# Optimization experiments

Measured on AMD Instinct MI355X. Metric: run time of the kernel, lower is better.

The kernel has to match this reference:

```python
import jax, jax.numpy as jnp
import numpy as np

INPUT_DIM, LATENT_DIM, HIDDEN_DIM, BATCH = 1024, 128, 1024, 32768


def setup_inputs() -> dict:
    key = jax.random.key(0)
    ks = jax.random.split(key, 12)
    s = 0.02
    x = (jax.random.uniform(ks[0], (BATCH, INPUT_DIM)) < 0.5).astype(jnp.float32)  # binary data
    eps = jax.random.normal(ks[1], (BATCH, LATENT_DIM), dtype=jnp.float32)
    return {
        "x": x,
        "eps": eps,
        "We1": jax.random.normal(ks[2], (INPUT_DIM, HIDDEN_DIM)) * s,
        "be1": jnp.zeros((HIDDEN_DIM,), jnp.float32),
        "Wmu": jax.random.normal(ks[3], (HIDDEN_DIM, LATENT_DIM)) * s,
        "bmu": jnp.zeros((LATENT_DIM,), jnp.float32),
        "Wls": jax.random.normal(ks[4], (HIDDEN_DIM, LATENT_DIM)) * s,
        "bls": jnp.zeros((LATENT_DIM,), jnp.float32),
        "Wd1": jax.random.normal(ks[5], (LATENT_DIM, HIDDEN_DIM)) * s,
        "bd1": jnp.zeros((HIDDEN_DIM,), jnp.float32),
        "Wd2": jax.random.normal(ks[6], (HIDDEN_DIM, INPUT_DIM)) * s,
        "bd2": jnp.zeros((INPUT_DIM,), jnp.float32),
    }


def reference(x, eps, We1, be1, Wmu, bmu, Wls, bls, Wd1, bd1, Wd2, bd2):
    # Encoder: one hidden ReLU layer, mu / logsigma heads
    h = jax.nn.relu(x @ We1 + be1)                      # [B, H]
    mu = h @ Wmu + bmu                                  # [B, L]
    logsigma = h @ Wls + bls                            # [B, L]
    # Reparameterization: z = sigma * eps + mu (vectorized diag(exp(logsigma)) @ eps)
    z = mu + jnp.exp(logsigma) * eps                    # [B, L]
    # Decoder: one hidden ReLU layer, sigmoid Bernoulli params
    hd = jax.nn.relu(z @ Wd1 + bd1)                     # [B, H]
    theta = jax.nn.sigmoid(hd @ Wd2 + bd2)              # [B, D]
    # Bernoulli log-likelihood: sum_j log(theta^x * (1-theta)^(1-x))
    log_px = jnp.sum(x * jnp.log(theta) + (1.0 - x) * jnp.log1p(-theta), axis=-1)  # [B]
    # KL(q||N(0,I)) = 0.5 * sum(sigma^2 + mu^2 - log(sigma^2) - 1)
    kl = 0.5 * jnp.sum(jnp.exp(2.0 * logsigma) + mu * mu - 2.0 * logsigma - 1.0, axis=-1)  # [B]
    return log_px - kl                                  # elbo_mc [B]
```

## Files before the change

kernel.cpp:

```cpp
#include <hip/hip_runtime.h>
#include <cstdint>
#include <cstddef>


typedef __bf16 bf16x8 __attribute__((ext_vector_type(8)));
typedef float f32x4 __attribute__((ext_vector_type(4)));

__device__ __forceinline__ unsigned short f32_to_bf16(float f) {
  unsigned int u = __float_as_uint(f);
  u += 0x7fffu + ((u >> 16) & 1u);
  return (unsigned short)(u >> 16);
}

__global__ void cast_bf16_k(const float* __restrict__ in,
                            unsigned short* __restrict__ out, int n4) {
  int stride = gridDim.x * blockDim.x;
  for (int i = blockIdx.x * blockDim.x + threadIdx.x; i < n4; i += stride) {
    float4 v = reinterpret_cast<const float4*>(in)[i];
    ushort4 o = make_ushort4(f32_to_bf16(v.x), f32_to_bf16(v.y),
                             f32_to_bf16(v.z), f32_to_bf16(v.w));
    reinterpret_cast<ushort4*>(out)[i] = o;
  }
}

struct TransJob { const float* in; unsigned short* out; int K, N, blkEnd; };

__global__ void transpose_all_k(TransJob j0, TransJob j1, TransJob j2,
                                TransJob j3, TransJob j4) {
  __shared__ float tile[32][33];
  int bid = blockIdx.x;
  TransJob j; int base;
  if (bid < j0.blkEnd)      { j = j0; base = 0; }
  else if (bid < j1.blkEnd) { j = j1; base = j0.blkEnd; }
  else if (bid < j2.blkEnd) { j = j2; base = j1.blkEnd; }
  else if (bid < j3.blkEnd) { j = j3; base = j2.blkEnd; }
  else                      { j = j4; base = j3.blkEnd; }
  int local = bid - base;
  int gxN = j.N >> 5;
  int n0 = (local % gxN) * 32, k0 = (local / gxN) * 32;
  int tx = threadIdx.x, ty = threadIdx.y;
#pragma unroll
  for (int r = 0; r < 32; r += 8)
    tile[ty + r][tx] = j.in[(size_t)(k0 + ty + r) * j.N + n0 + tx];
  __syncthreads();
#pragma unroll
  for (int r = 0; r < 32; r += 8)
    j.out[(size_t)(n0 + ty + r) * j.K + k0 + tx] = f32_to_bf16(tile[tx][ty + r]);
}

__device__ __forceinline__ void gl_lds16(const unsigned short* g, unsigned short* l) {
  __builtin_amdgcn_global_load_lds(
      (__attribute__((address_space(1))) void*)g,
      (__attribute__((address_space(3))) void*)l, 16, 0, 0);
}

template <int EPI>
__global__ __launch_bounds__(512, 2) void gemm256(
    const unsigned short* __restrict__ A, const unsigned short* __restrict__ BT,
    int gx, int N, int K,
    const float* __restrict__ bias0,
    unsigned short* __restrict__ outb, float* __restrict__ outf,
    const unsigned short* __restrict__ xbf) {
  __shared__ __align__(16) unsigned short lds[2][2][256 * 64];

  const int tid = threadIdx.x;
  const int lane = tid & 63;
  const int wave = tid >> 6;
  const int wr = wave >> 2;
  const int wc = wave & 3;
  const int lm = lane & 15, lq = lane >> 4;
  const int sw = lm & 7;

  const int bid = blockIdx.x;
  const int xcd = bid & 7;
  const int t8 = bid >> 3;
  const int m0 = (xcd + 8 * (t8 / gx)) * 256;
  const int n0 = (t8 % gx) * 256;
  const int NT = K >> 6;

  const unsigned short* gpA[2];
  const unsigned short* gpB[2];
  int loA[2], loB[2];
#pragma unroll
  for (int r = 0; r < 2; ++r) {
    int c = tid + 512 * r, rl = c >> 3, q8 = c & 7;
    int rowA = (rl & 63) + ((rl >> 6) << 7);
    int rowB = (rl & 31) + ((rl >> 5) << 6);
    gpA[r] = A + (size_t)(m0 + rowA) * K + (q8 ^ (rowA & 7)) * 8;
    gpB[r] = BT + (size_t)(n0 + rowB) * K + (q8 ^ (rowB & 7)) * 8;
    loA[r] = rowA * 64 + q8 * 8;
    loB[r] = rowB * 64 + q8 * 8;
  }

  auto stage = [&](int kind, int buf, int kt) {
#pragma unroll
    for (int r = 0; r < 2; ++r) {
      if (kind == 0)      gl_lds16(gpA[r] + kt * 64,          &lds[buf][0][loA[r]]);
      else if (kind == 3) gl_lds16(gpA[r] + 64 * K + kt * 64, &lds[buf][0][loA[r] + 64 * 64]);
      else if (kind == 1) gl_lds16(gpB[r] + kt * 64,          &lds[buf][1][loB[r]]);
      else                gl_lds16(gpB[r] + 32 * K + kt * 64, &lds[buf][1][loB[r] + 32 * 64]);
    }
  };

  stage(0, 0, 0); stage(1, 0, 0); stage(2, 0, 0); stage(3, 0, 0);
  stage(0, 1, 1); stage(1, 1, 1); stage(2, 1, 1);
  asm volatile("s_waitcnt vmcnt(6)" ::: "memory");
  __builtin_amdgcn_s_barrier();

  f32x4 acc[8][4] = {};

  const int aRow = (wr * 128 + lm) * 64;
  const int bRow = (wc * 64 + lm) * 64;
  const int c0 = ((0 | lq) ^ sw) * 8;
  const int c1 = ((4 | lq) ^ sw) * 8;

  for (int t = 0; t < NT; ++t) {
    const int b = t & 1;
    const unsigned short* Ab = &lds[b][0][0];
    const unsigned short* Bb = &lds[b][1][0];
    bf16x8 af[4][2], bf1[2][2], bf2[2][2];

#pragma unroll
    for (int i = 0; i < 4; ++i) {
      af[i][0] = *reinterpret_cast<const bf16x8*>(Ab + aRow + i * 16 * 64 + c0);
      af[i][1] = *reinterpret_cast<const bf16x8*>(Ab + aRow + i * 16 * 64 + c1);
    }
#pragma unroll
    for (int j = 0; j < 2; ++j) {
      bf1[j][0] = *reinterpret_cast<const bf16x8*>(Bb + bRow + j * 16 * 64 + c0);
      bf1[j][1] = *reinterpret_cast<const bf16x8*>(Bb + bRow + j * 16 * 64 + c1);
    }
    if (t + 1 < NT) stage(3, (t + 1) & 1, t + 1);
    __builtin_amdgcn_s_barrier();
    asm volatile("s_waitcnt lgkmcnt(0)" ::: "memory");
    __builtin_amdgcn_s_setprio(1);
#pragma unroll
    for (int s = 0; s < 2; ++s)
#pragma unroll
      for (int i = 0; i < 4; ++i)
#pragma unroll
        for (int j = 0; j < 2; ++j)
          acc[i][j] = __builtin_amdgcn_mfma_f32_16x16x32_bf16(af[i][s], bf1[j][s], acc[i][j], 0, 0, 0);
    __builtin_amdgcn_s_setprio(0);
    __builtin_amdgcn_s_barrier();

#pragma unroll
    for (int j = 0; j < 2; ++j) {
      bf2[j][0] = *reinterpret_cast<const bf16x8*>(Bb + bRow + (j + 2) * 16 * 64 + c0);
      bf2[j][1] = *reinterpret_cast<const bf16x8*>(Bb + bRow + (j + 2) * 16 * 64 + c1);
    }
    if (t + 2 < NT) stage(0, b, t + 2);
    __builtin_amdgcn_s_barrier();
    asm volatile("s_waitcnt lgkmcnt(0)" ::: "memory");
    __builtin_amdgcn_s_setprio(1);
#pragma unroll
    for (int s = 0; s < 2; ++s)
#pragma unroll
      for (int i = 0; i < 4; ++i)
#pragma unroll
        for (int j = 0; j < 2; ++j)
          acc[i][j + 2] = __builtin_amdgcn_mfma_f32_16x16x32_bf16(af[i][s], bf2[j][s], acc[i][j + 2], 0, 0, 0);
    __builtin_amdgcn_s_setprio(0);
    __builtin_amdgcn_s_barrier();

#pragma unroll
    for (int i = 0; i < 4; ++i) {
      af[i][0] = *reinterpret_cast<const bf16x8*>(Ab + aRow + (64 + i * 16) * 64 + c0);
      af[i][1] = *reinterpret_cast<const bf16x8*>(Ab + aRow + (64 + i * 16) * 64 + c1);
    }
    if (t + 2 < NT) stage(1, b, t + 2);
    __builtin_amdgcn_s_barrier();
    asm volatile("s_waitcnt lgkmcnt(0)" ::: "memory");
    __builtin_amdgcn_s_setprio(1);
#pragma unroll
    for (int s = 0; s < 2; ++s)
#pragma unroll
      for (int i = 0; i < 4; ++i)
#pragma unroll
        for (int j = 0; j < 2; ++j)
          acc[i + 4][j] = __builtin_amdgcn_mfma_f32_16x16x32_bf16(af[i][s], bf1[j][s], acc[i + 4][j], 0, 0, 0);
    __builtin_amdgcn_s_setprio(0);
    __builtin_amdgcn_s_barrier();

    if (t + 2 < NT) stage(2, b, t + 2);
    __builtin_amdgcn_s_barrier();
    __builtin_amdgcn_s_setprio(1);
#pragma unroll
    for (int s = 0; s < 2; ++s)
#pragma unroll
      for (int i = 0; i < 4; ++i)
#pragma unroll
        for (int j = 0; j < 2; ++j)
          acc[i + 4][j + 2] = __builtin_amdgcn_mfma_f32_16x16x32_bf16(af[i][s], bf2[j][s], acc[i + 4][j + 2], 0, 0, 0);
    __builtin_amdgcn_s_setprio(0);
    if (t + 2 < NT)      { asm volatile("s_waitcnt vmcnt(6)" ::: "memory"); }
    else if (t + 1 < NT) { asm volatile("s_waitcnt vmcnt(0)" ::: "memory"); }
    __builtin_amdgcn_s_barrier();
  }

  if (EPI == 0) {
#pragma unroll
    for (int i = 0; i < 8; ++i)
#pragma unroll
      for (int j = 0; j < 4; ++j) {
        int col = n0 + wc * 64 + j * 16 + lm;
        float bias = bias0[col];
#pragma unroll
        for (int r = 0; r < 4; ++r) {
          int row = m0 + wr * 128 + i * 16 + lq * 4 + r;
          float v = acc[i][j][r] + bias;
          outb[(size_t)row * N + col] = f32_to_bf16(fmaxf(v, 0.f));
        }
      }
  } else {
#pragma unroll
    for (int i = 0; i < 8; ++i) {
      float rs[4] = {0.f, 0.f, 0.f, 0.f};
#pragma unroll
      for (int j = 0; j < 4; ++j) {
        int col = n0 + wc * 64 + j * 16 + lm;
        float bias = bias0[col];
#pragma unroll
        for (int r = 0; r < 4; ++r) {
          int row = m0 + wr * 128 + i * 16 + lq * 4 + r;
          float l = acc[i][j][r] + bias;
          unsigned short xb = xbf[(size_t)row * N + col];
          float tt = xb ? -l : l;
          float sp = fmaxf(tt, 0.f) + __logf(1.f + __expf(-fabsf(tt)));
          rs[r] -= sp;
        }
      }
#pragma unroll
      for (int off = 1; off < 16; off <<= 1)
#pragma unroll
        for (int r = 0; r < 4; ++r) rs[r] += __shfl_xor(rs[r], off, 64);
      if (lm == 0) {
#pragma unroll
        for (int r = 0; r < 4; ++r)
          atomicAdd(&outf[m0 + wr * 128 + i * 16 + lq * 4 + r], rs[r]);
      }
    }
  }
}

__global__ __launch_bounds__(256, 1) void gemm2_zkl(
    const unsigned short* __restrict__ A,
    const unsigned short* __restrict__ BT,
    int K,
    const float* __restrict__ bmu, const float* __restrict__ bls,
    const float* __restrict__ eps,
    unsigned short* __restrict__ z,
    float* __restrict__ out) {
  __shared__ __align__(16) unsigned short As[128 * 64];
  __shared__ __align__(16) unsigned short Bs[256 * 64];

  const int tid = threadIdx.x;
  const int lane = tid & 63;
  const int wave = tid >> 6;
  const int m0 = blockIdx.x * 128;
  const int lm = lane & 15, lq = lane >> 4;

  const unsigned short* agp[4];
  const unsigned short* bgp[8];
#pragma unroll
  for (int r = 0; r < 4; ++r) {
    int c = tid + 256 * r;
    int row = c >> 3, q = (c & 7) ^ (row & 7);
    agp[r] = A + (size_t)(m0 + row) * K + q * 8;
  }
#pragma unroll
  for (int r = 0; r < 8; ++r) {
    int c = tid + 256 * r;
    int row = c >> 3, q = (c & 7) ^ (row & 7);
    bgp[r] = BT + (size_t)row * K + q * 8;
  }
  const int sw = lm & 7;

  f32x4 acc[2][16] = {};

  for (int kt = 0; kt < K; kt += 64) {
#pragma unroll
    for (int r = 0; r < 4; ++r) gl_lds16(agp[r] + kt, As + (tid + 256 * r) * 8);
#pragma unroll
    for (int r = 0; r < 8; ++r) gl_lds16(bgp[r] + kt, Bs + (tid + 256 * r) * 8);
    __syncthreads();

#pragma unroll
    for (int s = 0; s < 2; ++s) {
      const int so = ((s << 2) | lq) ^ sw;
      bf16x8 af[2];
#pragma unroll
      for (int i = 0; i < 2; ++i)
        af[i] = *reinterpret_cast<const bf16x8*>(As + (wave * 32 + i * 16 + lm) * 64 + so * 8);
#pragma unroll
      for (int j = 0; j < 16; ++j) {
        bf16x8 b = *reinterpret_cast<const bf16x8*>(Bs + (j * 16 + lm) * 64 + so * 8);
        acc[0][j] = __builtin_amdgcn_mfma_f32_16x16x32_bf16(af[0], b, acc[0][j], 0, 0, 0);
        acc[1][j] = __builtin_amdgcn_mfma_f32_16x16x32_bf16(af[1], b, acc[1][j], 0, 0, 0);
      }
    }
    __syncthreads();
  }

#pragma unroll
  for (int i = 0; i < 2; ++i) {
    float kl[4] = {0.f, 0.f, 0.f, 0.f};
#pragma unroll
    for (int j = 0; j < 8; ++j) {
      int dim = j * 16 + lm;
      float bm = bmu[dim], bl = bls[dim];
#pragma unroll
      for (int r = 0; r < 4; ++r) {
        int row = m0 + wave * 32 + i * 16 + lq * 4 + r;
        float mu = acc[i][j][r] + bm;
        float ls = acc[i][j + 8][r] + bl;
        float e = eps[(size_t)row * 128 + dim];
        z[(size_t)row * 128 + dim] = f32_to_bf16(fmaf(__expf(ls), e, mu));
        kl[r] += 0.5f * (__expf(2.f * ls) + mu * mu - 2.f * ls - 1.f);
      }
    }
#pragma unroll
    for (int off = 1; off < 16; off <<= 1)
#pragma unroll
      for (int r = 0; r < 4; ++r) kl[r] += __shfl_xor(kl[r], off, 64);
    if (lm == 0) {
#pragma unroll
      for (int r = 0; r < 4; ++r)
        out[m0 + wave * 32 + i * 16 + lq * 4 + r] = -kl[r];
    }
  }
}

extern "C" void kernel_launch(void* const* d_in, const int* in_sizes, int n_in,
                              void* d_out, int out_size, void* d_ws, size_t ws_size,
                              hipStream_t stream) {
  const float* x   = (const float*)d_in[0];
  const float* eps = (const float*)d_in[1];
  const float* We1 = (const float*)d_in[2];
  const float* be1 = (const float*)d_in[3];
  const float* Wmu = (const float*)d_in[4];
  const float* bmu = (const float*)d_in[5];
  const float* Wls = (const float*)d_in[6];
  const float* bls = (const float*)d_in[7];
  const float* Wd1 = (const float*)d_in[8];
  const float* bd1 = (const float*)d_in[9];
  const float* Wd2 = (const float*)d_in[10];
  const float* bd2 = (const float*)d_in[11];
  float* out = (float*)d_out;

  const int B = 32768, D = 1024, H = 1024, L = 128;

  char* ws = (char*)d_ws;
  size_t off = 0;
  auto alloc = [&](size_t bytes) {
    void* p = ws + off;
    off += (bytes + 255) & ~(size_t)255;
    return p;
  };
  unsigned short* xbf  = (unsigned short*)alloc((size_t)B * D * 2);
  unsigned short* w1t  = (unsigned short*)alloc((size_t)H * D * 2);
  unsigned short* w2t  = (unsigned short*)alloc((size_t)256 * H * 2);
  unsigned short* wd1t = (unsigned short*)alloc((size_t)H * L * 2);
  unsigned short* wd2t = (unsigned short*)alloc((size_t)D * H * 2);
  unsigned short* h    = (unsigned short*)alloc((size_t)B * H * 2);
  unsigned short* z    = (unsigned short*)alloc((size_t)B * L * 2);
  unsigned short* hd   = h;

  cast_bf16_k<<<2048, 256, 0, stream>>>(x, xbf, B * D / 4);

  TransJob j0{We1, w1t, D, H, 1024};
  TransJob j1{Wmu, w2t, H, L, 1152};
  TransJob j2{Wls, w2t + 128 * H, H, L, 1280};
  TransJob j3{Wd1, wd1t, L, H, 1408};
  TransJob j4{Wd2, wd2t, H, D, 2432};
  transpose_all_k<<<2432, dim3(32, 8), 0, stream>>>(j0, j1, j2, j3, j4);

  gemm256<0><<<512, 512, 0, stream>>>(
      xbf, w1t, 4, H, D, be1, h, nullptr, nullptr);
  gemm2_zkl<<<B / 128, 256, 0, stream>>>(h, w2t, H, bmu, bls, eps, z, out);
  gemm256<0><<<512, 512, 0, stream>>>(
      z, wd1t, 4, H, L, bd1, hd, nullptr, nullptr);
  gemm256<2><<<512, 512, 0, stream>>>(
      hd, wd2t, 4, D, H, bd2, nullptr, out, xbf);

  (void)in_sizes; (void)n_in; (void)out_size; (void)ws_size;
}
```

Baseline: 435.5 us.

## Prefetch next-tile LDS fragments across stages and relax wait counts in GEMM loop

```diff
diff --git a/kernel.cpp b/kernel.cpp
--- a/kernel.cpp
+++ b/kernel.cpp
@@ -104,35 +104,88 @@
 
   stage(0, 0, 0); stage(1, 0, 0); stage(2, 0, 0); stage(3, 0, 0);
   stage(0, 1, 1); stage(1, 1, 1); stage(2, 1, 1);
-  asm volatile("s_waitcnt vmcnt(6)" ::: "memory");
+  asm volatile("s_waitcnt vmcnt(8)" ::: "memory");
   __builtin_amdgcn_s_barrier();
 
   f32x4 acc[8][4] = {};
+  bf16x8 aL[4][2], aH[4][2], b1[2][2], b2[2][2];
 
   const int aRow = (wr * 128 + lm) * 64;
   const int bRow = (wc * 64 + lm) * 64;
   const int c0 = ((0 | lq) ^ sw) * 8;
   const int c1 = ((4 | lq) ^ sw) * 8;
 
+  {
+    const unsigned short* A0 = &lds[0][0][0];
+    const unsigned short* B0 = &lds[0][1][0];
+#pragma unroll
+    for (int i = 0; i < 4; ++i) {
+      aL[i][0] = *reinterpret_cast<const bf16x8*>(A0 + aRow + i * 1024 + c0);
+      aL[i][1] = *reinterpret_cast<const bf16x8*>(A0 + aRow + i * 1024 + c1);
+    }
+#pragma unroll
+    for (int j = 0; j < 2; ++j) {
+      b1[j][0] = *reinterpret_cast<const bf16x8*>(B0 + bRow + j * 1024 + c0);
+      b1[j][1] = *reinterpret_cast<const bf16x8*>(B0 + bRow + j * 1024 + c1);
+    }
+  }
+
   for (int t = 0; t < NT; ++t) {
     const int b = t & 1;
     const unsigned short* Ab = &lds[b][0][0];
     const unsigned short* Bb = &lds[b][1][0];
-    bf16x8 af[4][2], bf1[2][2], bf2[2][2];
+    const unsigned short* An = &lds[b ^ 1][0][0];
+    const unsigned short* Bn = &lds[b ^ 1][1][0];
+    const bool deep = (t + 2) < NT;
+
+#pragma unroll
+    for (int j = 0; j < 2; ++j) {
+      b2[j][0] = *reinterpret_cast<const bf16x8*>(Bb + bRow + (j + 2) * 1024 + c0);
+      b2[j][1] = *reinterpret_cast<const bf16x8*>(Bb + bRow + (j + 2) * 1024 + c1);
+    }
+    if (t + 1 < NT) stage(3, b ^ 1, t + 1);
+    __builtin_amdgcn_s_barrier();
+    asm volatile("s_waitcnt lgkmcnt(4)" ::: "memory");
+    __builtin_amdgcn_sched_barrier(0);
+    __builtin_amdgcn_s_setprio(1);
+#pragma unroll
+    for (int s = 0; s < 2; ++s)
+#pragma unroll
+      for (int i = 0; i < 4; ++i)
+#pragma unroll
+        for (int j = 0; j < 2; ++j)
+          acc[i][j] = __builtin_amdgcn_mfma_f32_16x16x32_bf16(aL[i][s], b1[j][s], acc[i][j], 0, 0, 0);
+    __builtin_amdgcn_s_setprio(0);
+    if (deep) { asm volatile("s_waitcnt vmcnt(8)" ::: "memory"); }
+    else      { asm volatile("s_waitcnt vmcnt(0)" ::: "memory"); }
+    __builtin_amdgcn_s_barrier();
 
 #pragma unroll
     for (int i = 0; i < 4; ++i) {
-      af[i][0] = *reinterpret_cast<const bf16x8*>(Ab + aRow + i * 16 * 64 + c0);
-      af[i][1] = *reinterpret_cast<const bf16x8*>(Ab + aRow + i * 16 * 64 + c1);
-    }
-#pragma unroll
-    for (int j = 0; j < 2; ++j) {
-      bf1[j][0] = *reinterpret_cast<const bf16x8*>(Bb + bRow + j * 16 * 64 + c0);
-      bf1[j][1] = *reinterpret_cast<const bf16x8*>(Bb + bRow + j * 16 * 64 + c1);
-    }
-    if (t + 1 < NT) stage(3, (t + 1) & 1, t + 1);
+      aH[i][0] = *reinterpret_cast<const bf16x8*>(Ab + aRow + 4096 + i * 1024 + c0);
+      aH[i][1] = *reinterpret_cast<const bf16x8*>(Ab + aRow + 4096 + i * 1024 + c1);
+    }
+    if (t + 2 < NT) stage(0, b, t + 2);
+    __builtin_amdgcn_s_barrier();
+    asm volatile("s_waitcnt lgkmcnt(8)" ::: "memory");
+    __builtin_amdgcn_sched_barrier(0);
+    __builtin_amdgcn_s_setprio(1);
+#pragma unroll
+    for (int s = 0; s < 2; ++s)
+#pragma unroll
+      for (int i = 0; i < 4; ++i)
+#pragma unroll
+        for (int j = 0; j < 2; ++j)
+          acc[i][j + 2] = __builtin_amdgcn_mfma_f32_16x16x32_bf16(aL[i][s], b2[j][s], acc[i][j + 2], 0, 0, 0);
+    __builtin_amdgcn_s_setprio(0);
+    if (deep) { asm volatile("s_waitcnt vmcnt(8)" ::: "memory"); }
+    else      { asm volatile("s_waitcnt vmcnt(0)" ::: "memory"); }
+    __builtin_amdgcn_s_barrier();
+
+    if (t + 2 < NT) stage(1, b, t + 2);
     __builtin_amdgcn_s_barrier();
     asm volatile("s_waitcnt lgkmcnt(0)" ::: "memory");
+    __builtin_amdgcn_sched_barrier(0);
     __builtin_amdgcn_s_setprio(1);
 #pragma unroll
     for (int s = 0; s < 2; ++s)
@@ -140,18 +193,26 @@
       for (int i = 0; i < 4; ++i)
 #pragma unroll
         for (int j = 0; j < 2; ++j)
-          acc[i][j] = __builtin_amdgcn_mfma_f32_16x16x32_bf16(af[i][s], bf1[j][s], acc[i][j], 0, 0, 0);
+          acc[i + 4][j] = __builtin_amdgcn_mfma_f32_16x16x32_bf16(aH[i][s], b1[j][s], acc[i + 4][j], 0, 0, 0);
     __builtin_amdgcn_s_setprio(0);
-    __builtin_amdgcn_s_barrier();
-
-#pragma unroll
-    for (int j = 0; j < 2; ++j) {
-      bf2[j][0] = *reinterpret_cast<const bf16x8*>(Bb + bRow + (j + 2) * 16 * 64 + c0);
-      bf2[j][1] = *reinterpret_cast<const bf16x8*>(Bb + bRow + (j + 2) * 16 * 64 + c1);
-    }
-    if (t + 2 < NT) stage(0, b, t + 2);
-    __builtin_amdgcn_s_barrier();
-    asm volatile("s_waitcnt lgkmcnt(0)" ::: "memory");
+    if (deep) { asm volatile("s_waitcnt vmcnt(8)" ::: "memory"); }
+    else      { asm volatile("s_waitcnt vmcnt(0)" ::: "memory"); }
+    __builtin_amdgcn_s_barrier();
+
+    if (t + 1 < NT) {
+#pragma unroll
+      for (int i = 0; i < 4; ++i) {
+        aL[i][0] = *reinterpret_cast<const bf16x8*>(An + aRow + i * 1024 + c0);
+        aL[i][1] = *reinterpret_cast<const bf16x8*>(An + aRow + i * 1024 + c1);
+      }
+#pragma unroll
+      for (int j = 0; j < 2; ++j) {
+        b1[j][0] = *reinterpret_cast<const bf16x8*>(Bn + bRow + j * 1024 + c0);
+        b1[j][1] = *reinterpret_cast<const bf16x8*>(Bn + bRow + j * 1024 + c1);
+      }
+    }
+    if (t + 2 < NT) stage(2, b, t + 2);
+    __builtin_amdgcn_s_barrier();
     __builtin_amdgcn_s_setprio(1);
 #pragma unroll
     for (int s = 0; s < 2; ++s)
@@ -159,42 +220,10 @@
       for (int i = 0; i < 4; ++i)
 #pragma unroll
         for (int j = 0; j < 2; ++j)
-          acc[i][j + 2] = __builtin_amdgcn_mfma_f32_16x16x32_bf16(af[i][s], bf2[j][s], acc[i][j + 2], 0, 0, 0);
+          acc[i + 4][j + 2] = __builtin_amdgcn_mfma_f32_16x16x32_bf16(aH[i][s], b2[j][s], acc[i + 4][j + 2], 0, 0, 0);
     __builtin_amdgcn_s_setprio(0);
-    __builtin_amdgcn_s_barrier();
-
-#pragma unroll
-    for (int i = 0; i < 4; ++i) {
-      af[i][0] = *reinterpret_cast<const bf16x8*>(Ab + aRow + (64 + i * 16) * 64 + c0);
-      af[i][1] = *reinterpret_cast<const bf16x8*>(Ab + aRow + (64 + i * 16) * 64 + c1);
-    }
-    if (t + 2 < NT) stage(1, b, t + 2);
-    __builtin_amdgcn_s_barrier();
-    asm volatile("s_waitcnt lgkmcnt(0)" ::: "memory");
-    __builtin_amdgcn_s_setprio(1);
-#pragma unroll
-    for (int s = 0; s < 2; ++s)
-#pragma unroll
-      for (int i = 0; i < 4; ++i)
-#pragma unroll
-        for (int j = 0; j < 2; ++j)
-          acc[i + 4][j] = __builtin_amdgcn_mfma_f32_16x16x32_bf16(af[i][s], bf1[j][s], acc[i + 4][j], 0, 0, 0);
-    __builtin_amdgcn_s_setprio(0);
-    __builtin_amdgcn_s_barrier();
-
-    if (t + 2 < NT) stage(2, b, t + 2);
-    __builtin_amdgcn_s_barrier();
-    __builtin_amdgcn_s_setprio(1);
-#pragma unroll
-    for (int s = 0; s < 2; ++s)
-#pragma unroll
-      for (int i = 0; i < 4; ++i)
-#pragma unroll
-        for (int j = 0; j < 2; ++j)
-          acc[i + 4][j + 2] = __builtin_amdgcn_mfma_f32_16x16x32_bf16(af[i][s], bf2[j][s], acc[i + 4][j + 2], 0, 0, 0);
-    __builtin_amdgcn_s_setprio(0);
-    if (t + 2 < NT)      { asm volatile("s_waitcnt vmcnt(6)" ::: "memory"); }
-    else if (t + 1 < NT) { asm volatile("s_waitcnt vmcnt(0)" ::: "memory"); }
+    if (deep) { asm volatile("s_waitcnt vmcnt(8)" ::: "memory"); }
+    else      { asm volatile("s_waitcnt vmcnt(0)" ::: "memory"); }
     __builtin_amdgcn_s_barrier();
   }
 
```

Result: slower. 447.2 us (+2.7%).

## Fuse latent GEMM with decoder first layer; bit-pack x for likelihood epilogue

Applied to the files above, without the earlier changes.

```diff
diff --git a/kernel.cpp b/kernel.cpp
--- a/kernel.cpp
+++ b/kernel.cpp
@@ -13,13 +13,21 @@
 }
 
 __global__ void cast_bf16_k(const float* __restrict__ in,
-                            unsigned short* __restrict__ out, int n4) {
+                            unsigned short* __restrict__ out,
+                            unsigned short* __restrict__ xbit, int n4) {
   int stride = gridDim.x * blockDim.x;
   for (int i = blockIdx.x * blockDim.x + threadIdx.x; i < n4; i += stride) {
     float4 v = reinterpret_cast<const float4*>(in)[i];
     ushort4 o = make_ushort4(f32_to_bf16(v.x), f32_to_bf16(v.y),
                              f32_to_bf16(v.z), f32_to_bf16(v.w));
     reinterpret_cast<ushort4*>(out)[i] = o;
+    unsigned int nib = (v.x != 0.f ? 1u : 0u) | (v.y != 0.f ? 2u : 0u) |
+                       (v.z != 0.f ? 4u : 0u) | (v.w != 0.f ? 8u : 0u);
+    unsigned int n1 = __shfl_down(nib, 1, 64);
+    unsigned int n2 = __shfl_down(nib, 2, 64);
+    unsigned int n3 = __shfl_down(nib, 3, 64);
+    if ((threadIdx.x & 3) == 0)
+      xbit[i >> 2] = (unsigned short)(nib | (n1 << 4) | (n2 << 8) | (n3 << 12));
   }
 }
 
@@ -54,13 +62,13 @@
       (__attribute__((address_space(3))) void*)l, 16, 0, 0);
 }
 
-template <int EPI>
+template <int EPI, int TAG>
 __global__ __launch_bounds__(512, 2) void gemm256(
     const unsigned short* __restrict__ A, const unsigned short* __restrict__ BT,
     int gx, int N, int K,
     const float* __restrict__ bias0,
     unsigned short* __restrict__ outb, float* __restrict__ outf,
-    const unsigned short* __restrict__ xbf) {
+    const unsigned short* __restrict__ xbit) {
   __shared__ __align__(16) unsigned short lds[2][2][256 * 64];
 
   const int tid = threadIdx.x;
@@ -122,17 +130,18 @@
 
 #pragma unroll
     for (int i = 0; i < 4; ++i) {
-      af[i][0] = *reinterpret_cast<const bf16x8*>(Ab + aRow + i * 16 * 64 + c0);
-      af[i][1] = *reinterpret_cast<const bf16x8*>(Ab + aRow + i * 16 * 64 + c1);
+      af[i][0] = *reinterpret_cast<const bf16x8*>(Ab + aRow + i * 1024 + c0);
+      af[i][1] = *reinterpret_cast<const bf16x8*>(Ab + aRow + i * 1024 + c1);
     }
 #pragma unroll
     for (int j = 0; j < 2; ++j) {
-      bf1[j][0] = *reinterpret_cast<const bf16x8*>(Bb + bRow + j * 16 * 64 + c0);
-      bf1[j][1] = *reinterpret_cast<const bf16x8*>(Bb + bRow + j * 16 * 64 + c1);
+      bf1[j][0] = *reinterpret_cast<const bf16x8*>(Bb + bRow + j * 1024 + c0);
+      bf1[j][1] = *reinterpret_cast<const bf16x8*>(Bb + bRow + j * 1024 + c1);
     }
     if (t + 1 < NT) stage(3, (t + 1) & 1, t + 1);
     __builtin_amdgcn_s_barrier();
     asm volatile("s_waitcnt lgkmcnt(0)" ::: "memory");
+    __builtin_amdgcn_sched_barrier(0);
     __builtin_amdgcn_s_setprio(1);
 #pragma unroll
     for (int s = 0; s < 2; ++s)
@@ -146,12 +155,13 @@
 
 #pragma unroll
     for (int j = 0; j < 2; ++j) {
-      bf2[j][0] = *reinterpret_cast<const bf16x8*>(Bb + bRow + (j + 2) * 16 * 64 + c0);
-      bf2[j][1] = *reinterpret_cast<const bf16x8*>(Bb + bRow + (j + 2) * 16 * 64 + c1);
+      bf2[j][0] = *reinterpret_cast<const bf16x8*>(Bb + bRow + (j + 2) * 1024 + c0);
+      bf2[j][1] = *reinterpret_cast<const bf16x8*>(Bb + bRow + (j + 2) * 1024 + c1);
     }
     if (t + 2 < NT) stage(0, b, t + 2);
     __builtin_amdgcn_s_barrier();
     asm volatile("s_waitcnt lgkmcnt(0)" ::: "memory");
+    __builtin_amdgcn_sched_barrier(0);
     __builtin_amdgcn_s_setprio(1);
 #pragma unroll
     for (int s = 0; s < 2; ++s)
@@ -171,6 +181,7 @@
     if (t + 2 < NT) stage(1, b, t + 2);
     __builtin_amdgcn_s_barrier();
     asm volatile("s_waitcnt lgkmcnt(0)" ::: "memory");
+    __builtin_amdgcn_sched_barrier(0);
     __builtin_amdgcn_s_setprio(1);
 #pragma unroll
     for (int s = 0; s < 2; ++s)
@@ -213,6 +224,7 @@
         }
       }
   } else {
+    const int wpr = N >> 4;
 #pragma unroll
     for (int i = 0; i < 8; ++i) {
       float rs[4] = {0.f, 0.f, 0.f, 0.f};
@@ -220,12 +232,13 @@
       for (int j = 0; j < 4; ++j) {
         int col = n0 + wc * 64 + j * 16 + lm;
         float bias = bias0[col];
+        int w16 = (col >> 4);
 #pragma unroll
         for (int r = 0; r < 4; ++r) {
           int row = m0 + wr * 128 + i * 16 + lq * 4 + r;
           float l = acc[i][j][r] + bias;
-          unsigned short xb = xbf[(size_t)row * N + col];
-          float tt = xb ? -l : l;
+          unsigned short mask = xbit[(size_t)row * wpr + w16];
+          float tt = ((mask >> lm) & 1) ? -l : l;
           float sp = fmaxf(tt, 0.f) + __logf(1.f + __expf(-fabsf(tt)));
           rs[r] -= sp;
         }
@@ -243,22 +256,28 @@
   }
 }
 
-__global__ __launch_bounds__(256, 1) void gemm2_zkl(
-    const unsigned short* __restrict__ A,
+__global__ __launch_bounds__(256, 1) void latent_fused(
+    const unsigned short* A,
     const unsigned short* __restrict__ BT,
-    int K,
+    const unsigned short* __restrict__ WD1,
     const float* __restrict__ bmu, const float* __restrict__ bls,
+    const float* __restrict__ bd1,
     const float* __restrict__ eps,
-    unsigned short* __restrict__ z,
+    unsigned short* hd,
     float* __restrict__ out) {
-  __shared__ __align__(16) unsigned short As[128 * 64];
-  __shared__ __align__(16) unsigned short Bs[256 * 64];
-
+  __shared__ __align__(16) unsigned short smem[49152];
+  unsigned short* As  = smem;
+  unsigned short* Bs  = smem + 8192;
+  unsigned short* Bs2 = smem;
+  unsigned short* zs  = smem + 32768;
+
+  const int K = 1024;
   const int tid = threadIdx.x;
   const int lane = tid & 63;
   const int wave = tid >> 6;
   const int m0 = blockIdx.x * 128;
   const int lm = lane & 15, lq = lane >> 4;
+  const int sw = lm & 7;
 
   const unsigned short* agp[4];
   const unsigned short* bgp[8];
@@ -274,7 +293,6 @@
     int row = c >> 3, q = (c & 7) ^ (row & 7);
     bgp[r] = BT + (size_t)row * K + q * 8;
   }
-  const int sw = lm & 7;
 
   f32x4 acc[2][16] = {};
 
@@ -302,6 +320,17 @@
     __syncthreads();
   }
 
+  auto stage2 = [&](int nt) {
+#pragma unroll
+    for (int ri = 0; ri < 16; ++ri) {
+      int c = tid + 256 * ri;
+      int row = c >> 4, slot = c & 15;
+      int gc = slot ^ (row & 7);
+      gl_lds16(WD1 + (size_t)(nt * 256 + row) * 128 + gc * 8, Bs2 + c * 8);
+    }
+  };
+  stage2(0);
+
 #pragma unroll
   for (int i = 0; i < 2; ++i) {
     float kl[4] = {0.f, 0.f, 0.f, 0.f};
@@ -311,11 +340,14 @@
       float bm = bmu[dim], bl = bls[dim];
 #pragma unroll
       for (int r = 0; r < 4; ++r) {
-        int row = m0 + wave * 32 + i * 16 + lq * 4 + r;
+        int rowl = wave * 32 + i * 16 + lq * 4 + r;
         float mu = acc[i][j][r] + bm;
         float ls = acc[i][j + 8][r] + bl;
-        float e = eps[(size_t)row * 128 + dim];
-        z[(size_t)row * 128 + dim] = f32_to_bf16(fmaf(__expf(ls), e, mu));
+        float e = eps[(size_t)(m0 + rowl) * 128 + dim];
+        float zv = fmaf(__expf(ls), e, mu);
+        int chunk = (dim >> 3);
+        int slot = chunk ^ (rowl & 7);
+        zs[rowl * 128 + slot * 8 + (lm & 7)] = f32_to_bf16(zv);
         kl[r] += 0.5f * (__expf(2.f * ls) + mu * mu - 2.f * ls - 1.f);
       }
     }
@@ -328,6 +360,39 @@
       for (int r = 0; r < 4; ++r)
         out[m0 + wave * 32 + i * 16 + lq * 4 + r] = -kl[r];
     }
+  }
+
+  for (int nt = 0; nt < 4; ++nt) {
+    asm volatile("s_waitcnt vmcnt(0)" ::: "memory");
+    __syncthreads();
+    f32x4 acc2[2][16] = {};
+#pragma unroll
+    for (int ks = 0; ks < 4; ++ks) {
+      const int cks = (ks * 4 + lq) ^ (lm & 7);
+      bf16x8 a0 = *reinterpret_cast<const bf16x8*>(zs + (wave * 32 + lm) * 128 + cks * 8);
+      bf16x8 a1 = *reinterpret_cast<const bf16x8*>(zs + (wave * 32 + 16 + lm) * 128 + cks * 8);
+#pragma unroll
+      for (int j = 0; j < 16; ++j) {
+        bf16x8 b = *reinterpret_cast<const bf16x8*>(Bs2 + (j * 16 + lm) * 128 + cks * 8);
+        acc2[0][j] = __builtin_amdgcn_mfma_f32_16x16x32_bf16(a0, b, acc2[0][j], 0, 0, 0);
+        acc2[1][j] = __builtin_amdgcn_mfma_f32_16x16x32_bf16(a1, b, acc2[1][j], 0, 0, 0);
+      }
+    }
+    __syncthreads();
+    if (nt + 1 < 4) stage2(nt + 1);
+#pragma unroll
+    for (int i = 0; i < 2; ++i)
+#pragma unroll
+      for (int j = 0; j < 16; ++j) {
+        int col = nt * 256 + j * 16 + lm;
+        float bias = bd1[col];
+#pragma unroll
+        for (int r = 0; r < 4; ++r) {
+          int row = m0 + wave * 32 + i * 16 + lq * 4 + r;
+          float v = acc2[i][j][r] + bias;
+          hd[(size_t)row * 1024 + col] = f32_to_bf16(fmaxf(v, 0.f));
+        }
+      }
   }
 }
 
@@ -358,15 +423,15 @@
     return p;
   };
   unsigned short* xbf  = (unsigned short*)alloc((size_t)B * D * 2);
+  unsigned short* xbit = (unsigned short*)alloc((size_t)B * D / 8);
   unsigned short* w1t  = (unsigned short*)alloc((size_t)H * D * 2);
   unsigned short* w2t  = (unsigned short*)alloc((size_t)256 * H * 2);
   unsigned short* wd1t = (unsigned short*)alloc((size_t)H * L * 2);
   unsigned short* wd2t = (unsigned short*)alloc((size_t)D * H * 2);
   unsigned short* h    = (unsigned short*)alloc((size_t)B * H * 2);
-  unsigned short* z    = (unsigned short*)alloc((size_t)B * L * 2);
   unsigned short* hd   = h;
 
-  cast_bf16_k<<<2048, 256, 0, stream>>>(x, xbf, B * D / 4);
+  cast_bf16_k<<<2048, 256, 0, stream>>>(x, xbf, xbit, B * D / 4);
 
   TransJob j0{We1, w1t, D, H, 1024};
   TransJob j1{Wmu, w2t, H, L, 1152};
@@ -375,13 +440,12 @@
   TransJob j4{Wd2, wd2t, H, D, 2432};
   transpose_all_k<<<2432, dim3(32, 8), 0, stream>>>(j0, j1, j2, j3, j4);
 
-  gemm256<0><<<512, 512, 0, stream>>>(
+  gemm256<0, 1><<<512, 512, 0, stream>>>(
       xbf, w1t, 4, H, D, be1, h, nullptr, nullptr);
-  gemm2_zkl<<<B / 128, 256, 0, stream>>>(h, w2t, H, bmu, bls, eps, z, out);
-  gemm256<0><<<512, 512, 0, stream>>>(
-      z, wd1t, 4, H, L, bd1, hd, nullptr, nullptr);
-  gemm256<2><<<512, 512, 0, stream>>>(
-      hd, wd2t, 4, D, H, bd2, nullptr, out, xbf);
+  latent_fused<<<B / 128, 256, 0, stream>>>(
+      h, w2t, wd1t, bmu, bls, bd1, eps, hd, out);
+  gemm256<2, 4><<<512, 512, 0, stream>>>(
+      hd, wd2t, 4, D, H, bd2, nullptr, out, xbit);
 
   (void)in_sizes; (void)n_in; (void)out_size; (void)ws_size;
 }
```

After: 444.8 us. 2.1% more time.
